# Performance work log

Measured on AMD Instinct MI355X. Metric: run time of the kernel, lower is better.

The kernel has to match this reference:

```python
import jax, jax.numpy as jnp
import numpy as np

FEATURE_SIZES = [300, 1000, 1000, 500, 150, 12, 31, 30, 200, 50000, 50000, 20000, 100000]
# sections per table index i (from feature_sizes_dict -> feature_sections_dict in original)
SECTIONS = [(0, 1), (1, 2), (2, 3), (3, 4), (4, 5), (5, 6), (6, 7), (7, 10),
            (10, 24), (26, 28), (28, 30), (24, 26), (30, 45)]
N, F, E = 8192, 45, 256
_perm, _tbl = [], []
for _i, (_a, _b) in enumerate(SECTIONS):
    for _j in range(_a, _b):
        _perm.append(_j)
        _tbl.append(_i)
PERM = np.array(_perm)              # original Xi column for field position p (concat order)
TBL = np.array(_tbl)                # table index for field position p
OFFSETS = np.concatenate([[0], np.cumsum(FEATURE_SIZES)[:-1]]).astype(np.int32)
FIELD_OFF = OFFSETS[TBL]            # row offset into concatenated table per field position
TOTAL_V = int(np.sum(FEATURE_SIZES))  # 223273
VOCAB_COL = np.zeros(F, np.int32)
VOCAB_COL[PERM] = np.array(FEATURE_SIZES, np.int32)[TBL]  # per-column valid vocab for Xi


def setup_inputs() -> dict:
    key = jax.random.key(0)
    ks = jax.random.split(key, 10)
    Xi = jax.random.randint(ks[0], (N, F), 0, jnp.asarray(VOCAB_COL), dtype=jnp.int32)
    Xv = jax.random.uniform(ks[1], (N, F), dtype=jnp.float32)
    W1 = jax.random.normal(ks[2], (TOTAL_V, 1), dtype=jnp.float32) * 0.01
    W2 = jax.random.normal(ks[3], (TOTAL_V, E), dtype=jnp.float32) * 0.01
    bias = jax.random.normal(ks[4], (1,), dtype=jnp.float32)
    l1_w = jax.random.normal(ks[5], (32, F * E), dtype=jnp.float32) * 0.02
    l1_b = jnp.zeros((32,), jnp.float32)
    l2_w = jax.random.normal(ks[6], (32, 32), dtype=jnp.float32) * 0.02
    l2_b = jnp.zeros((32,), jnp.float32)
    return {"Xi": Xi, "Xv": Xv, "W1": W1, "W2": W2, "bias": bias,
            "l1_w": l1_w, "l1_b": l1_b, "bn1_g": jnp.ones((32,), jnp.float32),
            "bn1_b": jnp.zeros((32,), jnp.float32), "l2_w": l2_w, "l2_b": l2_b,
            "bn2_g": jnp.ones((32,), jnp.float32), "bn2_b": jnp.zeros((32,), jnp.float32)}


def _batchnorm(x, g, b, eps=1e-5):
    # training-mode BN: biased batch statistics (PyTorch normalization convention)
    m = x.mean(0)
    v = x.var(0)
    return (x - m) * jax.lax.rsqrt(v + eps) * g + b


def reference(Xi, Xv, W1, W2, bias, l1_w, l1_b, bn1_g, bn1_b, l2_w, l2_b, bn2_g, bn2_b):
    perm = jnp.asarray(PERM)
    foff = jnp.asarray(FIELD_OFF)
    idx = Xi[:, perm] + foff[None, :]          # (N, 45) rows into concatenated tables
    xv = Xv[:, perm]                            # (N, 45) values in concat order
    # first-order: scalar embedding * value per field
    fm_first = W1[idx, 0] * xv                  # (N, 45)
    # second-order: E-dim embedding * value per field
    e = W2[idx] * xv[:, :, None]                # (N, 45, E)
    s = e.sum(axis=1)                           # (N, E)
    fm_second = 0.5 * (s * s - (e * e).sum(axis=1))  # (N, E)
    # deep part (concat of per-field 2nd-order embs, in original loop order)
    deep = e.reshape(e.shape[0], -1)            # (N, 45*E)
    h = _batchnorm(deep @ l1_w.T + l1_b, bn1_g, bn1_b)
    h = _batchnorm(h @ l2_w.T + l2_b, bn2_g, bn2_b)  # (N, 32); no final num_classes linear in original
    return fm_first.sum(axis=1) + fm_second.sum(axis=1) + h.sum(axis=1) + bias  # (N,)
```

## Files before the change

### kernel.cpp

```cpp
#include <hip/hip_runtime.h>
#include <hip/hip_bf16.h>

#define NS 8192
#define NF 45
#define ED 256
#define L1K 11520
#define NH 32

typedef __attribute__((ext_vector_type(8))) short bf16x8;
typedef __attribute__((ext_vector_type(4))) float f32x4;
typedef __attribute__((ext_vector_type(4))) unsigned uint32x4;

__constant__ int c_perm[NF] = {
    0,1,2,3,4,5,6,7,8,9,
    10,11,12,13,14,15,16,17,18,19,20,21,22,23,
    26,27, 28,29, 24,25,
    30,31,32,33,34,35,36,37,38,39,40,41,42,43,44};
__constant__ int c_foff[NF] = {
    0,300,1300,2300,2800,2950,2962,2993,2993,2993,
    3023,3023,3023,3023,3023,3023,3023,3023,3023,3023,3023,3023,3023,3023,
    3223,3223, 53223,53223, 103223,103223,
    123223,123223,123223,123223,123223,123223,123223,123223,
    123223,123223,123223,123223,123223,123223,123223};

__device__ __forceinline__ short f2bf(float x) {
    unsigned u = __builtin_bit_cast(unsigned, x);
    u += 0x7fffu + ((u >> 16) & 1u);
    return (short)(u >> 16);
}

__device__ __forceinline__ unsigned pk_bf16(float a, float b) {
    unsigned r;
    asm("v_cvt_pk_bf16_f32 %0, %1, %2" : "=v"(r) : "v"(a), "v"(b));
    return r;
}

__global__ __launch_bounds__(256) void k_pack(const float* __restrict__ l1w,
                                              short* __restrict__ bfrag) {
    int t = blockIdx.x * 256 + threadIdx.x;
    if (t >= NF * 8192) return;
    int i  = t & 7;
    int l  = (t >> 3) & 63;
    int nt = (t >> 9) & 1;
    int ks = (t >> 10) & 7;
    int f  = t >> 13;
    int kout = nt * 16 + (l & 15);
    int col  = f * 256 + ks * 32 + (l >> 4) * 8 + i;
    bfrag[t] = f2bf(l1w[kout * L1K + col]);
}

__global__ __launch_bounds__(512, 2) void k_main(const float* __restrict__ W2,
                                                 const float* __restrict__ W1,
                                                 const int* __restrict__ Xi,
                                                 const float* __restrict__ Xv,
                                                 const short* __restrict__ bfrag,
                                                 float* __restrict__ h1h,
                                                 float* __restrict__ parth,
                                                 float* __restrict__ S1,
                                                 float* __restrict__ S2) {
    __shared__ int   s_idx[32 * NF];
    __shared__ float s_xv [32 * NF];
    __shared__ float s_red[8 * 32 * 33];
    __shared__ float s_q[8 * 32];
    __shared__ float s_fm1[32];
    __shared__ float s_h[32 * 33];

    const int tid = threadIdx.x;
    const int w   = tid >> 6;
    const int l   = tid & 63;
    const int m   = l & 15;
    const int g4  = l >> 4;
    const int n0  = blockIdx.x * 32;

    for (int t = tid; t < 32 * NF; t += 512) {
        int f = t % NF;
        int n = n0 + t / NF;
        int col = c_perm[f];
        s_idx[t] = Xi[n * NF + col] + c_foff[f];
        s_xv[t]  = Xv[n * NF + col];
    }
    __syncthreads();

    f32x4 acc00 = {0.f,0.f,0.f,0.f}, acc01 = {0.f,0.f,0.f,0.f};
    f32x4 acc10 = {0.f,0.f,0.f,0.f}, acc11 = {0.f,0.f,0.f,0.f};
    float sA0[8], sA1[8];
    #pragma unroll
    for (int i = 0; i < 8; ++i) { sA0[i] = 0.f; sA1[i] = 0.f; }
    float esq0 = 0.f, esq1 = 0.f, fm10 = 0.f, fm11 = 0.f;

    const short* bbase = bfrag + (size_t)w * 1024 + l * 8;
    const float* wbase = W2 + w * 32 + g4 * 8;
    const bool  isw0   = (w == 0);
    const int   mNF    = m * NF;
    const int   mNF1   = (m + 16) * NF;

#define LOADF(ff, A00_,A01_,A10_,A11_,B0_,B1_,XV0_,XV1_,W10_,W11_)  \
    do {                                                            \
        int i0_ = s_idx[mNF  + (ff)];                               \
        int i1_ = s_idx[mNF1 + (ff)];                               \
        XV0_ = s_xv[mNF  + (ff)];                                   \
        XV1_ = s_xv[mNF1 + (ff)];                                   \
        const float* p0_ = wbase + (size_t)i0_ * ED;                \
        const float* p1_ = wbase + (size_t)i1_ * ED;                \
        A00_ = *(const f32x4*)(p0_);  A01_ = *(const f32x4*)(p0_ + 4); \
        A10_ = *(const f32x4*)(p1_);  A11_ = *(const f32x4*)(p1_ + 4); \
        const short* bp_ = bbase + (size_t)(ff) * 8192;             \
        B0_ = *(const bf16x8*)(bp_);                                \
        B1_ = *(const bf16x8*)(bp_ + 512);                          \
        W10_ = isw0 ? W1[i0_] : 0.f;                                \
        W11_ = isw0 ? W1[i1_] : 0.f;                                \
    } while (0)

#define COMPG(A0_,A1_,B0_,B1_,XV_,SA_,ESQ_,ACC0_,ACC1_,FM_,W1R_)    \
    do {                                                            \
        float e0=A0_.x*XV_, e1=A0_.y*XV_, e2=A0_.z*XV_, e3=A0_.w*XV_; \
        float e4=A1_.x*XV_, e5=A1_.y*XV_, e6=A1_.z*XV_, e7=A1_.w*XV_; \
        SA_[0]+=e0; SA_[1]+=e1; SA_[2]+=e2; SA_[3]+=e3;             \
        SA_[4]+=e4; SA_[5]+=e5; SA_[6]+=e6; SA_[7]+=e7;             \
        ESQ_ += e0*e0; ESQ_ += e1*e1; ESQ_ += e2*e2; ESQ_ += e3*e3; \
        ESQ_ += e4*e4; ESQ_ += e5*e5; ESQ_ += e6*e6; ESQ_ += e7*e7; \
        uint32x4 au_;                                               \
        au_.x = pk_bf16(e0,e1);  au_.y = pk_bf16(e2,e3);            \
        au_.z = pk_bf16(e4,e5);  au_.w = pk_bf16(e6,e7);            \
        bf16x8 Af_ = __builtin_bit_cast(bf16x8, au_);               \
        ACC0_ = __builtin_amdgcn_mfma_f32_16x16x32_bf16(Af_, B0_, ACC0_, 0,0,0); \
        ACC1_ = __builtin_amdgcn_mfma_f32_16x16x32_bf16(Af_, B1_, ACC1_, 0,0,0); \
        FM_ += W1R_ * XV_;                                          \
    } while (0)

#define COMPF(A00_,A01_,A10_,A11_,B0_,B1_,XV0_,XV1_,W10_,W11_)      \
    do {                                                            \
        COMPG(A00_,A01_,B0_,B1_,XV0_,sA0,esq0,acc00,acc01,fm10,W10_); \
        COMPG(A10_,A11_,B0_,B1_,XV1_,sA1,esq1,acc10,acc11,fm11,W11_); \
    } while (0)

    f32x4  A00a,A01a,A10a,A11a, A00b,A01b,A10b,A11b;
    f32x4  A00c,A01c,A10c,A11c, A00d,A01d,A10d,A11d;
    bf16x8 B0a,B1a, B0b,B1b, B0c,B1c, B0d,B1d;
    float  XV0a,XV1a, XV0b,XV1b, XV0c,XV1c, XV0d,XV1d;
    float  W10a,W11a, W10b,W11b, W10c,W11c, W10d,W11d;

    LOADF(0, A00a,A01a,A10a,A11a,B0a,B1a,XV0a,XV1a,W10a,W11a);
    LOADF(1, A00b,A01b,A10b,A11b,B0b,B1b,XV0b,XV1b,W10b,W11b);
    LOADF(2, A00c,A01c,A10c,A11c,B0c,B1c,XV0c,XV1c,W10c,W11c);
    LOADF(3, A00d,A01d,A10d,A11d,B0d,B1d,XV0d,XV1d,W10d,W11d);

    for (int f = 0; f + 7 < NF; f += 4) {
        COMPF(A00a,A01a,A10a,A11a,B0a,B1a,XV0a,XV1a,W10a,W11a);
        LOADF(f + 4, A00a,A01a,A10a,A11a,B0a,B1a,XV0a,XV1a,W10a,W11a);
        COMPF(A00b,A01b,A10b,A11b,B0b,B1b,XV0b,XV1b,W10b,W11b);
        LOADF(f + 5, A00b,A01b,A10b,A11b,B0b,B1b,XV0b,XV1b,W10b,W11b);
        COMPF(A00c,A01c,A10c,A11c,B0c,B1c,XV0c,XV1c,W10c,W11c);
        LOADF(f + 6, A00c,A01c,A10c,A11c,B0c,B1c,XV0c,XV1c,W10c,W11c);
        COMPF(A00d,A01d,A10d,A11d,B0d,B1d,XV0d,XV1d,W10d,W11d);
        LOADF(f + 7, A00d,A01d,A10d,A11d,B0d,B1d,XV0d,XV1d,W10d,W11d);
    }
    COMPF(A00a,A01a,A10a,A11a,B0a,B1a,XV0a,XV1a,W10a,W11a);
    LOADF(44, A00a,A01a,A10a,A11a,B0a,B1a,XV0a,XV1a,W10a,W11a);
    COMPF(A00b,A01b,A10b,A11b,B0b,B1b,XV0b,XV1b,W10b,W11b);
    COMPF(A00c,A01c,A10c,A11c,B0c,B1c,XV0c,XV1c,W10c,W11c);
    COMPF(A00d,A01d,A10d,A11d,B0d,B1d,XV0d,XV1d,W10d,W11d);
    COMPF(A00a,A01a,A10a,A11a,B0a,B1a,XV0a,XV1a,W10a,W11a);

#undef LOADF
#undef COMPG
#undef COMPF

    float q0 = -esq0, q1 = -esq1;
    #pragma unroll
    for (int i = 0; i < 8; ++i) { q0 += sA0[i] * sA0[i]; q1 += sA1[i] * sA1[i]; }
    q0 += __shfl_xor(q0, 16);  q0 += __shfl_xor(q0, 32);
    q1 += __shfl_xor(q1, 16);  q1 += __shfl_xor(q1, 32);
    if (l < 16) {
        s_q[w * 32 + m]      = q0;
        s_q[w * 32 + 16 + m] = q1;
        if (w == 0) { s_fm1[m] = fm10; s_fm1[16 + m] = fm11; }
    }

    #pragma unroll
    for (int r = 0; r < 4; ++r) {
        s_red[w * 1056 + (g4 * 4 + r) * 33 +      m] = acc00[r];
        s_red[w * 1056 + (g4 * 4 + r) * 33 + 16 + m] = acc01[r];
        s_red[w * 1056 + (16 + g4 * 4 + r) * 33 +      m] = acc10[r];
        s_red[w * 1056 + (16 + g4 * 4 + r) * 33 + 16 + m] = acc11[r];
    }
    __syncthreads();

    for (int t = tid; t < 1024; t += 512) {
        int s = t >> 5, j = t & 31;
        float v = 0.f;
        #pragma unroll
        for (int ww = 0; ww < 8; ++ww) v += s_red[ww * 1056 + s * 33 + j];
        h1h[(size_t)n0 * NH + t] = v;
        s_h[s * 33 + j] = v;
    }
    if (tid < 32) {
        float fm2 = 0.f;
        #pragma unroll
        for (int ww = 0; ww < 8; ++ww) fm2 += s_q[ww * 32 + tid];
        parth[n0 + tid] = s_fm1[tid] + 0.5f * fm2;
    }
    __syncthreads();

    {
        const int j  = tid >> 4;
        const int kk = (tid & 15) << 1;
        float p0 = 0.f, p1 = 0.f;
        #pragma unroll 8
        for (int s = 0; s < 32; ++s) {
            float hj = s_h[s * 33 + j];
            p0 += hj * s_h[s * 33 + kk];
            p1 += hj * s_h[s * 33 + kk + 1];
        }
        atomicAdd(&S2[j * NH + kk],     p0);
        atomicAdd(&S2[j * NH + kk + 1], p1);
        if (tid < 32) {
            float s1 = 0.f;
            #pragma unroll 8
            for (int s = 0; s < 32; ++s) s1 += s_h[s * 33 + tid];
            atomicAdd(&S1[tid], s1);
        }
    }
}

__global__ __launch_bounds__(256) void k_coef(const float* __restrict__ S1,
                                              const float* __restrict__ S2,
                                              const float* __restrict__ g1,
                                              const float* __restrict__ l2w,
                                              const float* __restrict__ g2,
                                              const float* __restrict__ b2,
                                              const float* __restrict__ bias,
                                              float* __restrict__ cvec,
                                              float* __restrict__ k0out) {
    __shared__ float m1[NH], d1[NH], g2r2[NH], csh[NH];
    __shared__ float s2s[NH * NH];
    const int t = threadIdx.x;
    const float invN = 1.f / (float)NS;
    for (int i = t; i < NH * NH; i += 256) s2s[i] = S2[i];
    __syncthreads();
    if (t < NH) {
        float mm = S1[t] * invN;
        float v1 = s2s[t * NH + t] * invN - mm * mm;
        m1[t] = mm;
        d1[t] = g1[t] * rsqrtf(v1 + 1e-5f);
    }
    __syncthreads();
    if (t < NH) {
        float aw[NH];
        float p = 0.f;
        for (int j = 0; j < NH; ++j) { aw[j] = l2w[t * NH + j] * d1[j]; p += aw[j] * m1[j]; }
        float v2 = 0.f;
        for (int j = 0; j < NH; ++j) {
            float acc = 0.f;
            for (int j2 = 0; j2 < NH; ++j2) acc += aw[j2] * s2s[j * NH + j2];
            v2 += aw[j] * acc;
        }
        v2 = v2 * invN - p * p;
        g2r2[t] = g2[t] * rsqrtf(v2 + 1e-5f);
    }
    __syncthreads();
    if (t < NH) {
        float s = 0.f;
        for (int k = 0; k < NH; ++k) s += g2r2[k] * l2w[k * NH + t];
        float c = d1[t] * s;
        csh[t] = c;
        cvec[t] = c;
    }
    __syncthreads();
    if (t == 0) {
        float k0 = bias[0];
        for (int k = 0; k < NH; ++k) k0 += b2[k];
        for (int j = 0; j < NH; ++j) k0 -= csh[j] * m1[j];
        k0out[0] = k0;
    }
}

__global__ __launch_bounds__(256) void k_final(const float* __restrict__ h1h,
                                               const float* __restrict__ parth,
                                               const float* __restrict__ cvec,
                                               const float* __restrict__ k0p,
                                               float* __restrict__ out) {
    __shared__ float c[NH];
    __shared__ float k0s;
    const int t = threadIdx.x;
    if (t < NH) c[t] = cvec[t];
    if (t == 0) k0s = k0p[0];
    __syncthreads();
    const int n = blockIdx.x * 256 + t;
    const f32x4* hp0 = (const f32x4*)(h1h + (size_t)n * NH);
    float dot = 0.f;
    #pragma unroll
    for (int q = 0; q < 8; ++q) {
        f32x4 h0 = hp0[q];
        dot += h0.x * c[q * 4]     + h0.y * c[q * 4 + 1]
             + h0.z * c[q * 4 + 2] + h0.w * c[q * 4 + 3];
    }
    out[n] = parth[n] + dot + k0s;
}

extern "C" void kernel_launch(void* const* d_in, const int* in_sizes, int n_in,
                              void* d_out, int out_size, void* d_ws, size_t ws_size,
                              hipStream_t stream) {
    const int*   Xi   = (const int*)  d_in[0];
    const float* Xv   = (const float*)d_in[1];
    const float* W1   = (const float*)d_in[2];
    const float* W2   = (const float*)d_in[3];
    const float* bias = (const float*)d_in[4];
    const float* l1w  = (const float*)d_in[5];
    const float* g1   = (const float*)d_in[7];
    const float* l2w  = (const float*)d_in[9];
    const float* g2   = (const float*)d_in[11];
    const float* b2   = (const float*)d_in[12];
    float* out = (float*)d_out;

    char* ws = (char*)d_ws;
    short* bfrag = (short*)ws;
    float* h1h   = (float*)(ws + (size_t)368640 * 2);
    float* parth = h1h + (size_t)NS * NH;
    float* S1    = parth + NS;
    float* S2    = S1 + NH;
    float* cvec  = S2 + NH * NH;
    float* k0p   = cvec + NH;

    hipMemsetAsync(S1, 0, (NH + NH * NH) * sizeof(float), stream);
    k_pack <<<(NF * 8192 + 255) / 256, 256, 0, stream>>>(l1w, bfrag);
    k_main <<<NS / 32, 512, 0, stream>>>(W2, W1, Xi, Xv, bfrag, h1h, parth, S1, S2);
    k_coef <<<1, 256, 0, stream>>>(S1, S2, g1, l2w, g2, b2, bias, cvec, k0p);
    k_final<<<NS / 256, 256, 0, stream>>>(h1h, parth, cvec, k0p, out);
}
```

Before: 363.2 us.

## Fuse pack, main, coef and final kernels into one cooperative kernel

Merges the weight-packing, main gather/GEMM, BN-coefficient and final-output kernels into a single cooperative launch that uses grid-wide syncs between phases. The h1 and partial results stay in shared memory instead of going to global memory, and the separate memset and three extra launches are removed. Each block now recomputes the small BN coefficient step redundantly. The two grid barriers add synchronisation cost and require all 256 blocks to be co-resident.

```diff
diff --git a/kernel.cpp b/kernel.cpp
--- a/kernel.cpp
+++ b/kernel.cpp
@@ -1,5 +1,8 @@
 #include <hip/hip_runtime.h>
 #include <hip/hip_bf16.h>
+#include <hip/hip_cooperative_groups.h>
+
+namespace cg = cooperative_groups;
 
 #define NS 8192
 #define NF 45
@@ -35,35 +38,30 @@
     return r;
 }
 
-__global__ __launch_bounds__(256) void k_pack(const float* __restrict__ l1w,
-                                              short* __restrict__ bfrag) {
-    int t = blockIdx.x * 256 + threadIdx.x;
-    if (t >= NF * 8192) return;
-    int i  = t & 7;
-    int l  = (t >> 3) & 63;
-    int nt = (t >> 9) & 1;
-    int ks = (t >> 10) & 7;
-    int f  = t >> 13;
-    int kout = nt * 16 + (l & 15);
-    int col  = f * 256 + ks * 32 + (l >> 4) * 8 + i;
-    bfrag[t] = f2bf(l1w[kout * L1K + col]);
-}
-
-__global__ __launch_bounds__(512, 2) void k_main(const float* __restrict__ W2,
-                                                 const float* __restrict__ W1,
-                                                 const int* __restrict__ Xi,
-                                                 const float* __restrict__ Xv,
-                                                 const short* __restrict__ bfrag,
-                                                 float* __restrict__ h1h,
-                                                 float* __restrict__ parth,
-                                                 float* __restrict__ S1,
-                                                 float* __restrict__ S2) {
+__global__ __launch_bounds__(512, 2) void k_fused(
+        const float* __restrict__ W2,  const float* __restrict__ W1,
+        const int*   __restrict__ Xi,  const float* __restrict__ Xv,
+        const float* __restrict__ l1w,
+        const float* __restrict__ g1,  const float* __restrict__ l2w,
+        const float* __restrict__ g2,  const float* __restrict__ b2,
+        const float* __restrict__ bias,
+        short* __restrict__ bfrag,
+        float* __restrict__ S1,
+        float* __restrict__ S2,
+        float* __restrict__ out) {
+
+    cg::grid_group grid = cg::this_grid();
+
     __shared__ int   s_idx[32 * NF];
     __shared__ float s_xv [32 * NF];
     __shared__ float s_red[8 * 32 * 33];
     __shared__ float s_q[8 * 32];
     __shared__ float s_fm1[32];
     __shared__ float s_h[32 * 33];
+    __shared__ float s_parth[32];
+    __shared__ float m1[NH], d1[NH], g2r2[NH], csh[NH];
+    __shared__ float s2s[NH * NH];
+    __shared__ float k0sh;
 
     const int tid = threadIdx.x;
     const int w   = tid >> 6;
@@ -71,6 +69,22 @@
     const int m   = l & 15;
     const int g4  = l >> 4;
     const int n0  = blockIdx.x * 32;
+
+    for (int t = blockIdx.x * 512 + tid; t < NF * 8192; t += 256 * 512) {
+        int i  = t & 7;
+        int ll = (t >> 3) & 63;
+        int nt = (t >> 9) & 1;
+        int ks = (t >> 10) & 7;
+        int f  = t >> 13;
+        int kout = nt * 16 + (ll & 15);
+        int col  = f * 256 + ks * 32 + (ll >> 4) * 8 + i;
+        bfrag[t] = f2bf(l1w[kout * L1K + col]);
+    }
+    if (blockIdx.x == 0) {
+        for (int t = tid; t < NH + NH * NH; t += 512) S1[t] = 0.f;
+    }
+    __threadfence();
+    grid.sync();
 
     for (int t = tid; t < 32 * NF; t += 512) {
         int f = t % NF;
@@ -191,14 +205,13 @@
         float v = 0.f;
         #pragma unroll
         for (int ww = 0; ww < 8; ++ww) v += s_red[ww * 1056 + s * 33 + j];
-        h1h[(size_t)n0 * NH + t] = v;
         s_h[s * 33 + j] = v;
     }
     if (tid < 32) {
         float fm2 = 0.f;
         #pragma unroll
         for (int ww = 0; ww < 8; ++ww) fm2 += s_q[ww * 32 + tid];
-        parth[n0 + tid] = s_fm1[tid] + 0.5f * fm2;
+        s_parth[tid] = s_fm1[tid] + 0.5f * fm2;
     }
     __syncthreads();
 
@@ -221,81 +234,58 @@
             atomicAdd(&S1[tid], s1);
         }
     }
-}
-
-__global__ __launch_bounds__(256) void k_coef(const float* __restrict__ S1,
-                                              const float* __restrict__ S2,
-                                              const float* __restrict__ g1,
-                                              const float* __restrict__ l2w,
-                                              const float* __restrict__ g2,
-                                              const float* __restrict__ b2,
-                                              const float* __restrict__ bias,
-                                              float* __restrict__ cvec,
-                                              float* __restrict__ k0out) {
-    __shared__ float m1[NH], d1[NH], g2r2[NH], csh[NH];
-    __shared__ float s2s[NH * NH];
-    const int t = threadIdx.x;
+    __threadfence();
+    grid.sync();
+
     const float invN = 1.f / (float)NS;
-    for (int i = t; i < NH * NH; i += 256) s2s[i] = S2[i];
-    __syncthreads();
-    if (t < NH) {
-        float mm = S1[t] * invN;
-        float v1 = s2s[t * NH + t] * invN - mm * mm;
-        m1[t] = mm;
-        d1[t] = g1[t] * rsqrtf(v1 + 1e-5f);
-    }
-    __syncthreads();
-    if (t < NH) {
+    for (int i = tid; i < NH * NH; i += 512) s2s[i] = S2[i];
+    __syncthreads();
+    if (tid < NH) {
+        float mm = S1[tid] * invN;
+        float v1 = s2s[tid * NH + tid] * invN - mm * mm;
+        m1[tid] = mm;
+        d1[tid] = g1[tid] * rsqrtf(v1 + 1e-5f);
+    }
+    __syncthreads();
+    if (tid < NH) {
         float aw[NH];
         float p = 0.f;
-        for (int j = 0; j < NH; ++j) { aw[j] = l2w[t * NH + j] * d1[j]; p += aw[j] * m1[j]; }
+        #pragma unroll
+        for (int j = 0; j < NH; ++j) { aw[j] = l2w[tid * NH + j] * d1[j]; p += aw[j] * m1[j]; }
         float v2 = 0.f;
         for (int j = 0; j < NH; ++j) {
             float acc = 0.f;
+            #pragma unroll 8
             for (int j2 = 0; j2 < NH; ++j2) acc += aw[j2] * s2s[j * NH + j2];
             v2 += aw[j] * acc;
         }
         v2 = v2 * invN - p * p;
-        g2r2[t] = g2[t] * rsqrtf(v2 + 1e-5f);
-    }
-    __syncthreads();
-    if (t < NH) {
+        g2r2[tid] = g2[tid] * rsqrtf(v2 + 1e-5f);
+    }
+    __syncthreads();
+    if (tid < NH) {
         float s = 0.f;
-        for (int k = 0; k < NH; ++k) s += g2r2[k] * l2w[k * NH + t];
-        float c = d1[t] * s;
-        csh[t] = c;
-        cvec[t] = c;
-    }
-    __syncthreads();
-    if (t == 0) {
+        #pragma unroll
+        for (int k = 0; k < NH; ++k) s += g2r2[k] * l2w[k * NH + tid];
+        csh[tid] = d1[tid] * s;
+    }
+    __syncthreads();
+    if (tid == 0) {
         float k0 = bias[0];
+        #pragma unroll
         for (int k = 0; k < NH; ++k) k0 += b2[k];
+        #pragma unroll
         for (int j = 0; j < NH; ++j) k0 -= csh[j] * m1[j];
-        k0out[0] = k0;
-    }
-}
-
-__global__ __launch_bounds__(256) void k_final(const float* __restrict__ h1h,
-                                               const float* __restrict__ parth,
-                                               const float* __restrict__ cvec,
-                                               const float* __restrict__ k0p,
-                                               float* __restrict__ out) {
-    __shared__ float c[NH];
-    __shared__ float k0s;
-    const int t = threadIdx.x;
-    if (t < NH) c[t] = cvec[t];
-    if (t == 0) k0s = k0p[0];
-    __syncthreads();
-    const int n = blockIdx.x * 256 + t;
-    const f32x4* hp0 = (const f32x4*)(h1h + (size_t)n * NH);
-    float dot = 0.f;
-    #pragma unroll
-    for (int q = 0; q < 8; ++q) {
-        f32x4 h0 = hp0[q];
-        dot += h0.x * c[q * 4]     + h0.y * c[q * 4 + 1]
-             + h0.z * c[q * 4 + 2] + h0.w * c[q * 4 + 3];
-    }
-    out[n] = parth[n] + dot + k0s;
+        k0sh = k0;
+    }
+    __syncthreads();
+
+    if (tid < 32) {
+        float dot = 0.f;
+        #pragma unroll
+        for (int j = 0; j < NH; ++j) dot += csh[j] * s_h[tid * 33 + j];
+        out[n0 + tid] = s_parth[tid] + dot + k0sh;
+    }
 }
 
 extern "C" void kernel_launch(void* const* d_in, const int* in_sizes, int n_in,
@@ -315,16 +305,13 @@
 
     char* ws = (char*)d_ws;
     short* bfrag = (short*)ws;
-    float* h1h   = (float*)(ws + (size_t)368640 * 2);
-    float* parth = h1h + (size_t)NS * NH;
-    float* S1    = parth + NS;
+    float* S1    = (float*)(ws + 737280);
     float* S2    = S1 + NH;
-    float* cvec  = S2 + NH * NH;
-    float* k0p   = cvec + NH;
-
-    hipMemsetAsync(S1, 0, (NH + NH * NH) * sizeof(float), stream);
-    k_pack <<<(NF * 8192 + 255) / 256, 256, 0, stream>>>(l1w, bfrag);
-    k_main <<<NS / 32, 512, 0, stream>>>(W2, W1, Xi, Xv, bfrag, h1h, parth, S1, S2);
-    k_coef <<<1, 256, 0, stream>>>(S1, S2, g1, l2w, g2, b2, bias, cvec, k0p);
-    k_final<<<NS / 256, 256, 0, stream>>>(h1h, parth, cvec, k0p, out);
+
+    void* kargs[] = {
+        (void*)&W2, (void*)&W1, (void*)&Xi, (void*)&Xv, (void*)&l1w,
+        (void*)&g1, (void*)&l2w, (void*)&g2, (void*)&b2, (void*)&bias,
+        (void*)&bfrag, (void*)&S1, (void*)&S2, (void*)&out };
+    hipLaunchCooperativeKernel((const void*)k_fused, dim3(256), dim3(512),
+                               kargs, 0, stream);
 }
```

New measurement: 496.7 us. +36.8%, slower.
